# Kernel optimization log

Hardware: AMD Instinct MI355X
Metric: run time of the kernel (lower is better)

## Reference

```python
import jax, jax.numpy as jnp
import numpy as np

N_NODES = 100000
N_EDGES = 3200000


def gcn_conv(x, src, dst, ew, W, b, num_nodes):
    """PyG GCNConv: h = x@W; out[dst] += norm * h[src]; norm = d^-1/2[src]*w*d^-1/2[dst].
    src/dst/ew must already include self-loops (weight 1)."""
    h = x @ W  # [N, F_out]
    deg = jax.ops.segment_sum(ew, dst, num_segments=num_nodes)  # weighted in-degree
    dinv = jnp.where(deg > 0, jax.lax.rsqrt(deg), 0.0)
    norm = dinv[src] * ew * dinv[dst]  # [E]
    msg = h[src] * norm[:, None]  # [E, F_out] gather + scale
    out = jax.ops.segment_sum(msg, dst, num_segments=num_nodes)  # scatter-add
    return out + b


def setup_inputs() -> dict:
    key = jax.random.key(0)
    k1, k2, k3, k4, k5 = jax.random.split(key, 5)
    x = jax.random.normal(k1, (N_NODES, 35), dtype=jnp.float32)
    edge_index = jax.random.randint(k2, (2, N_EDGES), 0, N_NODES, dtype=jnp.int64)
    edge_weight = jax.random.uniform(k3, (N_EDGES,), dtype=jnp.float32)
    W1 = jax.random.normal(k4, (35, 64), dtype=jnp.float32) * (1.0 / np.sqrt(35))
    b1 = jnp.zeros((64,), dtype=jnp.float32)
    W2 = jax.random.normal(k5, (64, 2), dtype=jnp.float32) * (1.0 / np.sqrt(64))
    b2 = jnp.zeros((2,), dtype=jnp.float32)
    return {"x": x, "edge_index": edge_index, "edge_weight": edge_weight,
            "W1": W1, "b1": b1, "W2": W2, "b2": b2}


def reference(x, edge_index, edge_weight, W1, b1, W2, b2):
    n = x.shape[0]
    # add self-loops with weight 1 (PyG default fill_value=1), static shapes
    loop = jnp.arange(n, dtype=edge_index.dtype)
    src = jnp.concatenate([edge_index[0], loop])
    dst = jnp.concatenate([edge_index[1], loop])
    ew = jnp.concatenate([edge_weight, jnp.ones((n,), dtype=edge_weight.dtype)])

    h = jax.nn.relu(gcn_conv(x, src, dst, ew, W1, b1, n))
    h = gcn_conv(h, src, dst, ew, W2, b2, n)
    return jax.nn.log_softmax(h, axis=1)
```

## Files before the change

### kernel.cpp

```cpp
#include <hip/hip_runtime.h>
#include <hip/hip_fp16.h>
#include <math.h>

#define FIN 35
#define F1  64
#define BSZ 256
#define MAXNB 1024
#define CHUNK 16384
#define SCAP 12288

__global__ void k_hist(const int* __restrict__ dst, int* __restrict__ cmat,
                       int E, int NB, int NCHUNK) {
    __shared__ int h[MAXNB];
    int c = blockIdx.x, t = threadIdx.x;
    for (int i = t; i < NB; i += 256) h[i] = 0;
    __syncthreads();
    int e0 = c * CHUNK, e1 = min(e0 + CHUNK, E);
    bool al = ((size_t)(dst + e0) & 15) == 0;
    int nv = al ? ((e1 - e0) >> 2) : 0;
    const int4* d4 = (const int4*)(dst + e0);
    for (int i = t; i < nv; i += 256) {
        int4 v = d4[i];
        atomicAdd(&h[v.x >> 8], 1); atomicAdd(&h[v.y >> 8], 1);
        atomicAdd(&h[v.z >> 8], 1); atomicAdd(&h[v.w >> 8], 1);
    }
    for (int e = e0 + (nv << 2) + t; e < e1; e += 256) atomicAdd(&h[dst[e] >> 8], 1);
    __syncthreads();
    for (int i = t; i < NB; i += 256) cmat[(size_t)i * NCHUNK + c] = h[i];
}

__global__ void k_scan_row(int* __restrict__ cmat, int* __restrict__ rsum, int NCHUNK) {
    __shared__ int s[256];
    int b = blockIdx.x, t = threadIdx.x;
    int v = (t < NCHUNK) ? cmat[(size_t)b * NCHUNK + t] : 0;
    s[t] = v;
    __syncthreads();
    #pragma unroll
    for (int off = 1; off < 256; off <<= 1) {
        int tv = (t >= off) ? s[t - off] : 0;
        __syncthreads();
        s[t] += tv;
        __syncthreads();
    }
    if (t < NCHUNK) cmat[(size_t)b * NCHUNK + t] = s[t] - v;
    if (t == 255) rsum[b] = s[255];
}

__global__ void k_scan_buck(const int* __restrict__ rsum, int* __restrict__ bbase,
                            int* __restrict__ boff, int NB, int E) {
    __shared__ int s[512];
    int t = threadIdx.x;
    int v = (t < NB) ? rsum[t] : 0;
    s[t] = v;
    __syncthreads();
    #pragma unroll
    for (int off = 1; off < 512; off <<= 1) {
        int tv = (t >= off) ? s[t - off] : 0;
        __syncthreads();
        s[t] += tv;
        __syncthreads();
    }
    if (t < NB) {
        int excl = s[t] - v;
        bbase[t] = excl;
        boff[t] = excl;
    }
    if (t == 0) boff[NB] = E;
}

__global__ void k_place(const int* __restrict__ src, const int* __restrict__ dst,
                        const float* __restrict__ ew, const int* __restrict__ cmat,
                        const int* __restrict__ bbase,
                        int2* __restrict__ recs, int E, int NB, int NCHUNK) {
    __shared__ int base[MAXNB];
    __shared__ int cur[MAXNB];
    int c = blockIdx.x, t = threadIdx.x;
    for (int i = t; i < NB; i += 256) {
        base[i] = cmat[(size_t)i * NCHUNK + c] + bbase[i];
        cur[i] = 0;
    }
    __syncthreads();
    int e0 = c * CHUNK, e1 = min(e0 + CHUNK, E);
    bool al = (((size_t)(dst + e0) | (size_t)(src + e0) | (size_t)(ew + e0)) & 15) == 0;
    int nv = al ? ((e1 - e0) >> 2) : 0;
    const int4*   s4 = (const int4*)(src + e0);
    const int4*   d4 = (const int4*)(dst + e0);
    const float4* w4 = (const float4*)(ew + e0);
    for (int i = t; i < nv; i += 256) {
        int4   sv = s4[i];
        int4   dv = d4[i];
        float4 wv = w4[i];
        int b, r;
        b = dv.x >> 8; r = atomicAdd(&cur[b], 1);
        recs[base[b] + r] = make_int2(sv.x | ((dv.x & 255) << 24), __float_as_int(wv.x));
        b = dv.y >> 8; r = atomicAdd(&cur[b], 1);
        recs[base[b] + r] = make_int2(sv.y | ((dv.y & 255) << 24), __float_as_int(wv.y));
        b = dv.z >> 8; r = atomicAdd(&cur[b], 1);
        recs[base[b] + r] = make_int2(sv.z | ((dv.z & 255) << 24), __float_as_int(wv.z));
        b = dv.w >> 8; r = atomicAdd(&cur[b], 1);
        recs[base[b] + r] = make_int2(sv.w | ((dv.w & 255) << 24), __float_as_int(wv.w));
    }
    for (int e = e0 + (nv << 2) + t; e < e1; e += 256) {
        int d = dst[e];
        int b = d >> 8;
        int r = atomicAdd(&cur[b], 1);
        recs[base[b] + r] = make_int2(src[e] | ((d & 255) << 24), __float_as_int(ew[e]));
    }
}

__global__ __launch_bounds__(1024) void k_sort(
        const int* __restrict__ boff, const int2* __restrict__ recs_in,
        int2* __restrict__ recs_out, int* __restrict__ row_ptr,
        float* __restrict__ dinv, int n) {
    extern __shared__ int2 lrec[];
    __shared__ int   hcnt[BSZ];
    __shared__ int   hoff[BSZ];
    __shared__ float dsum[BSZ];
    int b = blockIdx.x, t = threadIdx.x;
    if (t < BSZ) { hcnt[t] = 0; dsum[t] = 1.0f; }
    __syncthreads();
    int s0 = boff[b], s1 = boff[b + 1];
    int cnt = s1 - s0;
    int nm = min(cnt, SCAP);
    for (int i = t; i < nm; i += 1024) {
        int2 rc = recs_in[s0 + i];
        lrec[i] = rc;
        int dl = ((unsigned)rc.x) >> 24;
        atomicAdd(&hcnt[dl], 1);
        atomicAdd(&dsum[dl], __int_as_float(rc.y));
    }
    for (int i = SCAP + t; i < cnt; i += 1024) {
        int2 rc = recs_in[s0 + i];
        int dl = ((unsigned)rc.x) >> 24;
        atomicAdd(&hcnt[dl], 1);
        atomicAdd(&dsum[dl], __int_as_float(rc.y));
    }
    __syncthreads();
    int v = 0;
    if (t < BSZ) { v = hcnt[t]; hoff[t] = v; }
    __syncthreads();
    #pragma unroll
    for (int off = 1; off < BSZ; off <<= 1) {
        int tv = 0;
        if (t < BSZ && t >= off) tv = hoff[t - off];
        __syncthreads();
        if (t < BSZ) hoff[t] += tv;
        __syncthreads();
    }
    if (t < BSZ) {
        int excl = hoff[t] - v;
        int node = b * BSZ + t;
        if (node < n) {
            row_ptr[node] = s0 + excl;
            dinv[node] = rsqrtf(dsum[t]);
            if (node == n - 1) row_ptr[n] = s1;
        }
        hcnt[t] = excl;
    }
    __syncthreads();
    for (int i = t; i < nm; i += 1024) {
        int2 rc = lrec[i];
        int dl = ((unsigned)rc.x) >> 24;
        int pos = atomicAdd(&hcnt[dl], 1);
        recs_out[s0 + pos] = make_int2(rc.x & 0xFFFFFF, rc.y);
    }
    for (int i = SCAP + t; i < cnt; i += 1024) {
        int2 rc = recs_in[s0 + i];
        int dl = ((unsigned)rc.x) >> 24;
        int pos = atomicAdd(&hcnt[dl], 1);
        recs_out[s0 + pos] = make_int2(rc.x & 0xFFFFFF, rc.y);
    }
}

__global__ void k_gemm1(const float* __restrict__ x, const float* __restrict__ W1,
                        const float* __restrict__ dinv, __half* __restrict__ g1, int n) {
    __shared__ float W1s[FIN * F1];
    __shared__ float xs[64 * FIN];
    int t = threadIdx.x;
    for (int i = t; i < FIN * F1; i += 256) W1s[i] = W1[i];
    int row0 = blockIdx.x * 64;
    int nrows = min(64, n - row0);
    for (int i = t; i < nrows * FIN; i += 256) xs[i] = x[(size_t)row0 * FIN + i];
    __syncthreads();
    int wave = t >> 6, f = t & 63;
    for (int rl = wave; rl < nrows; rl += 4) {
        float acc = 0.0f;
        #pragma unroll
        for (int k = 0; k < FIN; k++) acc += xs[rl * FIN + k] * W1s[k * F1 + f];
        int row = row0 + rl;
        g1[(size_t)row * F1 + f] = __float2half(acc * dinv[row]);
    }
}

__global__ void k_gather1(const int* __restrict__ rp, const int2* __restrict__ csr,
                          const __half* __restrict__ g1,
                          const float* __restrict__ dinv, const float* __restrict__ b1,
                          const float* __restrict__ W2, float* __restrict__ g2, int n) {
    int wid = (int)((blockIdx.x * (long long)blockDim.x + threadIdx.x) >> 6);
    int f = threadIdx.x & 63;
    if (wid >= n) return;
    int start = rp[wid], end = rp[wid + 1];
    float acc = 0.0f;
    int e = start;
    for (; e + 8 <= end; e += 8) {
        int2 r0 = csr[e],   r1 = csr[e+1], r2 = csr[e+2], r3 = csr[e+3];
        int2 r4 = csr[e+4], r5 = csr[e+5], r6 = csr[e+6], r7 = csr[e+7];
        float a0 = __half2float(g1[(size_t)r0.x * F1 + f]);
        float a1 = __half2float(g1[(size_t)r1.x * F1 + f]);
        float a2 = __half2float(g1[(size_t)r2.x * F1 + f]);
        float a3 = __half2float(g1[(size_t)r3.x * F1 + f]);
        float a4 = __half2float(g1[(size_t)r4.x * F1 + f]);
        float a5 = __half2float(g1[(size_t)r5.x * F1 + f]);
        float a6 = __half2float(g1[(size_t)r6.x * F1 + f]);
        float a7 = __half2float(g1[(size_t)r7.x * F1 + f]);
        acc += __int_as_float(r0.y) * a0; acc += __int_as_float(r1.y) * a1;
        acc += __int_as_float(r2.y) * a2; acc += __int_as_float(r3.y) * a3;
        acc += __int_as_float(r4.y) * a4; acc += __int_as_float(r5.y) * a5;
        acc += __int_as_float(r6.y) * a6; acc += __int_as_float(r7.y) * a7;
    }
    for (; e + 4 <= end; e += 4) {
        int2 r0 = csr[e], r1 = csr[e+1], r2 = csr[e+2], r3 = csr[e+3];
        float a0 = __half2float(g1[(size_t)r0.x * F1 + f]);
        float a1 = __half2float(g1[(size_t)r1.x * F1 + f]);
        float a2 = __half2float(g1[(size_t)r2.x * F1 + f]);
        float a3 = __half2float(g1[(size_t)r3.x * F1 + f]);
        acc += __int_as_float(r0.y) * a0; acc += __int_as_float(r1.y) * a1;
        acc += __int_as_float(r2.y) * a2; acc += __int_as_float(r3.y) * a3;
    }
    for (; e < end; e++) {
        int2 r = csr[e];
        acc += __int_as_float(r.y) * __half2float(g1[(size_t)r.x * F1 + f]);
    }
    float dv = dinv[wid];
    float h = dv * (acc + __half2float(g1[(size_t)wid * F1 + f])) + b1[f];
    h = h > 0.0f ? h : 0.0f;
    float2 w2v = ((const float2*)W2)[f];
    float z0 = h * w2v.x, z1 = h * w2v.y;
    #pragma unroll
    for (int off = 32; off > 0; off >>= 1) {
        z0 += __shfl_xor(z0, off, 64);
        z1 += __shfl_xor(z1, off, 64);
    }
    if (f == 0) {
        g2[(size_t)wid * 2 + 0] = dv * z0;
        g2[(size_t)wid * 2 + 1] = dv * z1;
    }
}

__global__ void k_gather2(const int* __restrict__ rp, const int2* __restrict__ csr,
                          const float* __restrict__ g2,
                          const float* __restrict__ dinv, const float* __restrict__ b2,
                          float* __restrict__ out, int n) {
    int wid = (int)((blockIdx.x * (long long)blockDim.x + threadIdx.x) >> 6);
    int lane = threadIdx.x & 63;
    if (wid >= n) return;
    int start = rp[wid], end = rp[wid + 1];
    float a0 = 0.0f, a1 = 0.0f;
    int e = start + lane;
    for (; e + 192 < end; e += 256) {
        int2 q0 = csr[e], q1 = csr[e + 64], q2 = csr[e + 128], q3 = csr[e + 192];
        float2 v0 = ((const float2*)g2)[q0.x];
        float2 v1 = ((const float2*)g2)[q1.x];
        float2 v2 = ((const float2*)g2)[q2.x];
        float2 v3 = ((const float2*)g2)[q3.x];
        a0 += __int_as_float(q0.y) * v0.x; a1 += __int_as_float(q0.y) * v0.y;
        a0 += __int_as_float(q1.y) * v1.x; a1 += __int_as_float(q1.y) * v1.y;
        a0 += __int_as_float(q2.y) * v2.x; a1 += __int_as_float(q2.y) * v2.y;
        a0 += __int_as_float(q3.y) * v3.x; a1 += __int_as_float(q3.y) * v3.y;
    }
    for (; e < end; e += 64) {
        int2 r = csr[e];
        float w = __int_as_float(r.y);
        float2 gv = ((const float2*)g2)[r.x];
        a0 += w * gv.x; a1 += w * gv.y;
    }
    #pragma unroll
    for (int off = 32; off > 0; off >>= 1) {
        a0 += __shfl_xor(a0, off, 64);
        a1 += __shfl_xor(a1, off, 64);
    }
    if (lane == 0) {
        float dv = dinv[wid];
        float2 sv = ((const float2*)g2)[wid];
        float z0 = dv * (a0 + sv.x) + b2[0];
        float z1 = dv * (a1 + sv.y) + b2[1];
        float m = fmaxf(z0, z1);
        float lse = m + logf(expf(z0 - m) + expf(z1 - m));
        ((float2*)out)[wid] = make_float2(z0 - lse, z1 - lse);
    }
}

extern "C" void kernel_launch(void* const* d_in, const int* in_sizes, int n_in,
                              void* d_out, int out_size, void* d_ws, size_t ws_size,
                              hipStream_t stream) {
    const float* x  = (const float*)d_in[0];
    const int*   ei = (const int*)d_in[1];
    const float* ew = (const float*)d_in[2];
    const float* W1 = (const float*)d_in[3];
    const float* b1 = (const float*)d_in[4];
    const float* W2 = (const float*)d_in[5];
    const float* b2 = (const float*)d_in[6];
    float* out = (float*)d_out;

    int n = in_sizes[0] / FIN;
    int E = in_sizes[2];
    const int* src = ei;
    const int* dst = ei + E;
    int NB = (n + BSZ - 1) / BSZ;
    int NCHUNK = (E + CHUNK - 1) / CHUNK;
    int M = NB * NCHUNK;

    char* ws = (char*)d_ws;
    size_t off = 0;
    auto alloc = [&](size_t bytes) -> void* {
        void* p = ws + off;
        off += (bytes + 15) & ~(size_t)15;
        return p;
    };
    int*    cmat    = (int*)   alloc((size_t)M * 4);
    int*    rsum    = (int*)   alloc((size_t)NB * 4);
    int*    bbase   = (int*)   alloc((size_t)NB * 4);
    int*    boff    = (int*)   alloc((size_t)(NB + 1) * 4);
    int*    row_ptr = (int*)   alloc((size_t)(n + 1) * 4);
    float*  dinv    = (float*) alloc((size_t)n * 4);
    int2*   recs_a  = (int2*)  alloc((size_t)E * 8);
    int2*   recs_b  = (int2*)  alloc((size_t)E * 8);
    __half* g1      = (__half*)alloc((size_t)n * F1 * 2);
    float*  g2      = (float*) alloc((size_t)n * 2 * 4);

    k_hist     <<<NCHUNK, 256, 0, stream>>>(dst, cmat, E, NB, NCHUNK);
    k_scan_row <<<NB, 256, 0, stream>>>(cmat, rsum, NCHUNK);
    k_scan_buck<<<1, 512, 0, stream>>>(rsum, bbase, boff, NB, E);
    k_place    <<<NCHUNK, 256, 0, stream>>>(src, dst, ew, cmat, bbase, recs_a, E, NB, NCHUNK);
    k_sort     <<<NB, 1024, SCAP * sizeof(int2), stream>>>(boff, recs_a, recs_b, row_ptr, dinv, n);
    k_gemm1    <<<(n + 63) / 64, 256, 0, stream>>>(x, W1, dinv, g1, n);
    k_gather1  <<<(n + 3) / 4, 256, 0, stream>>>(row_ptr, recs_b, g1, dinv, b1, W2, g2, n);
    k_gather2  <<<(n + 3) / 4, 256, 0, stream>>>(row_ptr, recs_b, g2, dinv, b2, out, n);
}
```

Measured before the change: 324.0 us.

## Halve sort bucket size, store pre-scaled source offsets, deepen gather unroll

Buckets shrink from 256 to 128 nodes, so the bucket count roughly doubles. That gives the sort kernel more blocks of 512 threads with a smaller shared-memory staging area, and the bucket scan is widened to 1024 threads to cover them. The sort now writes each source index pre-shifted into a byte offset into the fp16 feature rows. Both gather kernels then address memory directly: layer 1 uses the offset as is, and layer 2 shifts it right by 4. This removes the per-edge multiply, and layer-1 aggregation is unrolled to 16 edges to keep more loads in flight, at the cost of more register pressure.

```diff
diff --git a/kernel.cpp b/kernel.cpp
--- a/kernel.cpp
+++ b/kernel.cpp
@@ -4,10 +4,11 @@
 
 #define FIN 35
 #define F1  64
-#define BSZ 256
+#define BSZ 128
+#define BSH 7
 #define MAXNB 1024
 #define CHUNK 16384
-#define SCAP 12288
+#define SCAP 6144
 
 __global__ void k_hist(const int* __restrict__ dst, int* __restrict__ cmat,
                        int E, int NB, int NCHUNK) {
@@ -21,10 +22,10 @@
     const int4* d4 = (const int4*)(dst + e0);
     for (int i = t; i < nv; i += 256) {
         int4 v = d4[i];
-        atomicAdd(&h[v.x >> 8], 1); atomicAdd(&h[v.y >> 8], 1);
-        atomicAdd(&h[v.z >> 8], 1); atomicAdd(&h[v.w >> 8], 1);
-    }
-    for (int e = e0 + (nv << 2) + t; e < e1; e += 256) atomicAdd(&h[dst[e] >> 8], 1);
+        atomicAdd(&h[v.x >> BSH], 1); atomicAdd(&h[v.y >> BSH], 1);
+        atomicAdd(&h[v.z >> BSH], 1); atomicAdd(&h[v.w >> BSH], 1);
+    }
+    for (int e = e0 + (nv << 2) + t; e < e1; e += 256) atomicAdd(&h[dst[e] >> BSH], 1);
     __syncthreads();
     for (int i = t; i < NB; i += 256) cmat[(size_t)i * NCHUNK + c] = h[i];
 }
@@ -48,13 +49,13 @@
 
 __global__ void k_scan_buck(const int* __restrict__ rsum, int* __restrict__ bbase,
                             int* __restrict__ boff, int NB, int E) {
-    __shared__ int s[512];
+    __shared__ int s[1024];
     int t = threadIdx.x;
     int v = (t < NB) ? rsum[t] : 0;
     s[t] = v;
     __syncthreads();
     #pragma unroll
-    for (int off = 1; off < 512; off <<= 1) {
+    for (int off = 1; off < 1024; off <<= 1) {
         int tv = (t >= off) ? s[t - off] : 0;
         __syncthreads();
         s[t] += tv;
@@ -91,24 +92,24 @@
         int4   dv = d4[i];
         float4 wv = w4[i];
         int b, r;
-        b = dv.x >> 8; r = atomicAdd(&cur[b], 1);
-        recs[base[b] + r] = make_int2(sv.x | ((dv.x & 255) << 24), __float_as_int(wv.x));
-        b = dv.y >> 8; r = atomicAdd(&cur[b], 1);
-        recs[base[b] + r] = make_int2(sv.y | ((dv.y & 255) << 24), __float_as_int(wv.y));
-        b = dv.z >> 8; r = atomicAdd(&cur[b], 1);
-        recs[base[b] + r] = make_int2(sv.z | ((dv.z & 255) << 24), __float_as_int(wv.z));
-        b = dv.w >> 8; r = atomicAdd(&cur[b], 1);
-        recs[base[b] + r] = make_int2(sv.w | ((dv.w & 255) << 24), __float_as_int(wv.w));
+        b = dv.x >> BSH; r = atomicAdd(&cur[b], 1);
+        recs[base[b] + r] = make_int2(sv.x | ((dv.x & (BSZ-1)) << 24), __float_as_int(wv.x));
+        b = dv.y >> BSH; r = atomicAdd(&cur[b], 1);
+        recs[base[b] + r] = make_int2(sv.y | ((dv.y & (BSZ-1)) << 24), __float_as_int(wv.y));
+        b = dv.z >> BSH; r = atomicAdd(&cur[b], 1);
+        recs[base[b] + r] = make_int2(sv.z | ((dv.z & (BSZ-1)) << 24), __float_as_int(wv.z));
+        b = dv.w >> BSH; r = atomicAdd(&cur[b], 1);
+        recs[base[b] + r] = make_int2(sv.w | ((dv.w & (BSZ-1)) << 24), __float_as_int(wv.w));
     }
     for (int e = e0 + (nv << 2) + t; e < e1; e += 256) {
         int d = dst[e];
-        int b = d >> 8;
+        int b = d >> BSH;
         int r = atomicAdd(&cur[b], 1);
-        recs[base[b] + r] = make_int2(src[e] | ((d & 255) << 24), __float_as_int(ew[e]));
-    }
-}
-
-__global__ __launch_bounds__(1024) void k_sort(
+        recs[base[b] + r] = make_int2(src[e] | ((d & (BSZ-1)) << 24), __float_as_int(ew[e]));
+    }
+}
+
+__global__ __launch_bounds__(512) void k_sort(
         const int* __restrict__ boff, const int2* __restrict__ recs_in,
         int2* __restrict__ recs_out, int* __restrict__ row_ptr,
         float* __restrict__ dinv, int n) {
@@ -122,14 +123,14 @@
     int s0 = boff[b], s1 = boff[b + 1];
     int cnt = s1 - s0;
     int nm = min(cnt, SCAP);
-    for (int i = t; i < nm; i += 1024) {
+    for (int i = t; i < nm; i += 512) {
         int2 rc = recs_in[s0 + i];
         lrec[i] = rc;
         int dl = ((unsigned)rc.x) >> 24;
         atomicAdd(&hcnt[dl], 1);
         atomicAdd(&dsum[dl], __int_as_float(rc.y));
     }
-    for (int i = SCAP + t; i < cnt; i += 1024) {
+    for (int i = SCAP + t; i < cnt; i += 512) {
         int2 rc = recs_in[s0 + i];
         int dl = ((unsigned)rc.x) >> 24;
         atomicAdd(&hcnt[dl], 1);
@@ -158,17 +159,17 @@
         hcnt[t] = excl;
     }
     __syncthreads();
-    for (int i = t; i < nm; i += 1024) {
+    for (int i = t; i < nm; i += 512) {
         int2 rc = lrec[i];
         int dl = ((unsigned)rc.x) >> 24;
         int pos = atomicAdd(&hcnt[dl], 1);
-        recs_out[s0 + pos] = make_int2(rc.x & 0xFFFFFF, rc.y);
-    }
-    for (int i = SCAP + t; i < cnt; i += 1024) {
+        recs_out[s0 + pos] = make_int2((rc.x & 0xFFFFFF) << BSH, rc.y);
+    }
+    for (int i = SCAP + t; i < cnt; i += 512) {
         int2 rc = recs_in[s0 + i];
         int dl = ((unsigned)rc.x) >> 24;
         int pos = atomicAdd(&hcnt[dl], 1);
-        recs_out[s0 + pos] = make_int2(rc.x & 0xFFFFFF, rc.y);
+        recs_out[s0 + pos] = make_int2((rc.x & 0xFFFFFF) << BSH, rc.y);
     }
 }
 
@@ -199,37 +200,33 @@
     int wid = (int)((blockIdx.x * (long long)blockDim.x + threadIdx.x) >> 6);
     int f = threadIdx.x & 63;
     if (wid >= n) return;
+    const char* g1b = (const char*)g1 + f * 2;
     int start = rp[wid], end = rp[wid + 1];
     float acc = 0.0f;
     int e = start;
-    for (; e + 8 <= end; e += 8) {
-        int2 r0 = csr[e],   r1 = csr[e+1], r2 = csr[e+2], r3 = csr[e+3];
-        int2 r4 = csr[e+4], r5 = csr[e+5], r6 = csr[e+6], r7 = csr[e+7];
-        float a0 = __half2float(g1[(size_t)r0.x * F1 + f]);
-        float a1 = __half2float(g1[(size_t)r1.x * F1 + f]);
-        float a2 = __half2float(g1[(size_t)r2.x * F1 + f]);
-        float a3 = __half2float(g1[(size_t)r3.x * F1 + f]);
-        float a4 = __half2float(g1[(size_t)r4.x * F1 + f]);
-        float a5 = __half2float(g1[(size_t)r5.x * F1 + f]);
-        float a6 = __half2float(g1[(size_t)r6.x * F1 + f]);
-        float a7 = __half2float(g1[(size_t)r7.x * F1 + f]);
+    for (; e + 16 <= end; e += 16) {
+        float a[16];
+        int2 r[16];
+        #pragma unroll
+        for (int j = 0; j < 16; j++) r[j] = csr[e + j];
+        #pragma unroll
+        for (int j = 0; j < 16; j++)
+            a[j] = __half2float(*(const __half*)(g1b + (unsigned)r[j].x));
+        #pragma unroll
+        for (int j = 0; j < 16; j++) acc += __int_as_float(r[j].y) * a[j];
+    }
+    for (; e + 4 <= end; e += 4) {
+        int2 r0 = csr[e], r1 = csr[e+1], r2 = csr[e+2], r3 = csr[e+3];
+        float a0 = __half2float(*(const __half*)(g1b + (unsigned)r0.x));
+        float a1 = __half2float(*(const __half*)(g1b + (unsigned)r1.x));
+        float a2 = __half2float(*(const __half*)(g1b + (unsigned)r2.x));
+        float a3 = __half2float(*(const __half*)(g1b + (unsigned)r3.x));
         acc += __int_as_float(r0.y) * a0; acc += __int_as_float(r1.y) * a1;
         acc += __int_as_float(r2.y) * a2; acc += __int_as_float(r3.y) * a3;
-        acc += __int_as_float(r4.y) * a4; acc += __int_as_float(r5.y) * a5;
-        acc += __int_as_float(r6.y) * a6; acc += __int_as_float(r7.y) * a7;
-    }
-    for (; e + 4 <= end; e += 4) {
-        int2 r0 = csr[e], r1 = csr[e+1], r2 = csr[e+2], r3 = csr[e+3];
-        float a0 = __half2float(g1[(size_t)r0.x * F1 + f]);
-        float a1 = __half2float(g1[(size_t)r1.x * F1 + f]);
-        float a2 = __half2float(g1[(size_t)r2.x * F1 + f]);
-        float a3 = __half2float(g1[(size_t)r3.x * F1 + f]);
-        acc += __int_as_float(r0.y) * a0; acc += __int_as_float(r1.y) * a1;
-        acc += __int_as_float(r2.y) * a2; acc += __int_as_float(r3.y) * a3;
     }
     for (; e < end; e++) {
         int2 r = csr[e];
-        acc += __int_as_float(r.y) * __half2float(g1[(size_t)r.x * F1 + f]);
+        acc += __int_as_float(r.y) * __half2float(*(const __half*)(g1b + (unsigned)r.x));
     }
     float dv = dinv[wid];
     float h = dv * (acc + __half2float(g1[(size_t)wid * F1 + f])) + b1[f];
@@ -254,15 +251,16 @@
     int wid = (int)((blockIdx.x * (long long)blockDim.x + threadIdx.x) >> 6);
     int lane = threadIdx.x & 63;
     if (wid >= n) return;
+    const char* g2b = (const char*)g2;
     int start = rp[wid], end = rp[wid + 1];
     float a0 = 0.0f, a1 = 0.0f;
     int e = start + lane;
     for (; e + 192 < end; e += 256) {
         int2 q0 = csr[e], q1 = csr[e + 64], q2 = csr[e + 128], q3 = csr[e + 192];
-        float2 v0 = ((const float2*)g2)[q0.x];
-        float2 v1 = ((const float2*)g2)[q1.x];
-        float2 v2 = ((const float2*)g2)[q2.x];
-        float2 v3 = ((const float2*)g2)[q3.x];
+        float2 v0 = *(const float2*)(g2b + (((unsigned)q0.x) >> 4));
+        float2 v1 = *(const float2*)(g2b + (((unsigned)q1.x) >> 4));
+        float2 v2 = *(const float2*)(g2b + (((unsigned)q2.x) >> 4));
+        float2 v3 = *(const float2*)(g2b + (((unsigned)q3.x) >> 4));
         a0 += __int_as_float(q0.y) * v0.x; a1 += __int_as_float(q0.y) * v0.y;
         a0 += __int_as_float(q1.y) * v1.x; a1 += __int_as_float(q1.y) * v1.y;
         a0 += __int_as_float(q2.y) * v2.x; a1 += __int_as_float(q2.y) * v2.y;
@@ -271,7 +269,7 @@
     for (; e < end; e += 64) {
         int2 r = csr[e];
         float w = __int_as_float(r.y);
-        float2 gv = ((const float2*)g2)[r.x];
+        float2 gv = *(const float2*)(g2b + (((unsigned)r.x) >> 4));
         a0 += w * gv.x; a1 += w * gv.y;
     }
     #pragma unroll
@@ -330,9 +328,9 @@
 
     k_hist     <<<NCHUNK, 256, 0, stream>>>(dst, cmat, E, NB, NCHUNK);
     k_scan_row <<<NB, 256, 0, stream>>>(cmat, rsum, NCHUNK);
-    k_scan_buck<<<1, 512, 0, stream>>>(rsum, bbase, boff, NB, E);
+    k_scan_buck<<<1, 1024, 0, stream>>>(rsum, bbase, boff, NB, E);
     k_place    <<<NCHUNK, 256, 0, stream>>>(src, dst, ew, cmat, bbase, recs_a, E, NB, NCHUNK);
-    k_sort     <<<NB, 1024, SCAP * sizeof(int2), stream>>>(boff, recs_a, recs_b, row_ptr, dinv, n);
+    k_sort     <<<NB, 512, SCAP * sizeof(int2), stream>>>(boff, recs_a, recs_b, row_ptr, dinv, n);
     k_gemm1    <<<(n + 63) / 64, 256, 0, stream>>>(x, W1, dinv, g1, n);
     k_gather1  <<<(n + 3) / 4, 256, 0, stream>>>(row_ptr, recs_b, g1, dinv, b1, W2, g2, n);
     k_gather2  <<<(n + 3) / 4, 256, 0, stream>>>(row_ptr, recs_b, g2, dinv, b2, out, n);
```

Measured after the change: 342.8 us. 1.06x slower.
